# Kernel optimization log

Hardware: AMD Instinct MI355X
Metric: run time of the kernel (lower is better)

## Reference

```python
import jax, jax.numpy as jnp
import numpy as np

N_NODES = 10000
N_EDGES = 200000
STEPS = 2


def setup_inputs() -> dict:
    key = jax.random.key(0)
    ks = jax.random.split(key, 32)

    def w(k, shape):
        return jax.random.normal(k, shape, dtype=jnp.float32) * 0.05

    inp = {
        "x": jax.random.normal(ks[0], (N_NODES, 128), dtype=jnp.float32),
        "edge_attr": jax.random.normal(ks[1], (N_EDGES, 64), dtype=jnp.float32),
        "edge_index": jax.random.randint(ks[2], (2, N_EDGES), 0, N_NODES, dtype=jnp.int32),
        # node embedding MLP: 128 -> 128 -> 128 (ReLU after each, end_with_relu=True)
        "Wne1": w(ks[3], (128, 128)), "bne1": jnp.zeros((128,), jnp.float32),
        "Wne2": w(ks[4], (128, 128)), "bne2": jnp.zeros((128,), jnp.float32),
        # edge embedding MLP: 64 -> 128 -> 128
        "Wee1": w(ks[5], (64, 128)), "bee1": jnp.zeros((128,), jnp.float32),
        "Wee2": w(ks[6], (128, 128)), "bee2": jnp.zeros((128,), jnp.float32),
        # mlp_edge: (2*128*2 + 128*2)=768 -> 512 -> 128, ReLU after each
        "We1": w(ks[7], (768, 512)), "be1": jnp.zeros((512,), jnp.float32),
        "We2": w(ks[8], (512, 128)), "be2": jnp.zeros((128,), jnp.float32),
        # mlp_node: (128*2 + 128)=384 -> 128, ReLU
        "Wn1": w(ks[9], (384, 128)), "bn1": jnp.zeros((128,), jnp.float32),
        # update_mlp: 128 -> 128, ReLU
        "Wu": w(ks[10], (128, 128)), "bu": jnp.zeros((128,), jnp.float32),
        # node classification: 128 -> 128 (ReLU) -> 1
        "Wnc1": w(ks[11], (128, 128)), "bnc1": jnp.zeros((128,), jnp.float32),
        "Wnc2": w(ks[12], (128, 1)), "bnc2": jnp.zeros((1,), jnp.float32),
        # edge classification: 128 -> 128 (ReLU) -> 1
        "Wec1": w(ks[13], (128, 128)), "bec1": jnp.zeros((128,), jnp.float32),
        "Wec2": w(ks[14], (128, 1)), "bec2": jnp.zeros((1,), jnp.float32),
    }
    return inp


def reference(x, edge_attr, edge_index,
              Wne1, bne1, Wne2, bne2,
              Wee1, bee1, Wee2, bee2,
              We1, be1, We2, be2,
              Wn1, bn1, Wu, bu,
              Wnc1, bnc1, Wnc2, bnc2,
              Wec1, bec1, Wec2, bec2):
    relu = jax.nn.relu
    N = x.shape[0]
    j, i = edge_index[0], edge_index[1]  # j = source, i = target

    nf = relu(relu(x @ Wne1 + bne1) @ Wne2 + bne2)            # [N, 128]
    ef = relu(relu(edge_attr @ Wee1 + bee1) @ Wee2 + bee2)    # [E, 128]
    nf0, ef0 = nf, ef

    for _ in range(STEPS):
        # skip connections: concat initial features
        nfc = jnp.concatenate([nf0, nf], axis=1)   # [N, 256]
        efc = jnp.concatenate([ef0, ef], axis=1)   # [E, 256]
        x_i = nfc[i]                               # [E, 256] gather (target)
        x_j = nfc[j]                               # [E, 256] gather (source)
        # mlp_edge on [x_i, x_j, e_ij] -> new edge features [E, 128]
        e = relu(relu(jnp.concatenate([x_i, x_j, efc], axis=1) @ We1 + be1) @ We2 + be2)
        # message: mlp_node on [x_i, edge_attr] -> [E, 128]
        m = relu(jnp.concatenate([x_i, e], axis=1) @ Wn1 + bn1)
        # aggregate (add) messages at target nodes i
        agg = jax.ops.segment_sum(m, i, num_segments=N)       # [N, 128]
        # update MLP
        nf = relu(agg @ Wu + bu)
        ef = e

    preds_node = jnp.squeeze(relu(nf @ Wnc1 + bnc1) @ Wnc2 + bnc2)  # [N]
    preds_edge = jnp.squeeze(relu(ef @ Wec1 + bec1) @ Wec2 + bec2)  # [E]
    return (preds_edge, preds_node)
```

## Files before the change

### kernel.cpp

```cpp
#include <hip/hip_runtime.h>
#include <hip/hip_bf16.h>

#define N_NODES 10000
#define N_EDGES 200000
#define TE 32

typedef __attribute__((ext_vector_type(8))) short short8;
typedef __attribute__((ext_vector_type(4))) float f32x4;

static __device__ __forceinline__ ushort f2bf(float x) {
  union { __hip_bfloat16 h; ushort u; } v;
  v.h = __float2bfloat16(x);
  return v.u;
}
static __device__ __forceinline__ uint pk2bf(float lo, float hi) {
  union { __hip_bfloat162 h; uint u; } v;
  v.h = __float22bfloat162_rn(make_float2(lo, hi));
  return v.u;
}
static __device__ __forceinline__ float bf2f(ushort h) {
  union { uint u; float f; } v; v.u = ((uint)h) << 16;
  return v.f;
}

__device__ __forceinline__ void permute_job(
    const float* W, ushort* Wp, int o, int K, int N, int ld,
    int row0, int n0, int Ntot)
{
  if (o >= K * N) return;
  int k = o & 31;
  int n = (o >> 5) % N;
  int kt = o / (N * 32);
  Wp[(size_t)kt * Ntot * 32 + (size_t)(n0 + n) * 32 + k] =
      f2bf(W[(size_t)(row0 + kt * 32 + k) * ld + n]);
}

__global__ __launch_bounds__(256) void permute_all(
    const float* __restrict__ We1, const float* __restrict__ We2,
    const float* __restrict__ Wn1, const float* __restrict__ Wee1,
    const float* __restrict__ Wee2, const float* __restrict__ Wec1,
    ushort* __restrict__ Wsp, ushort* __restrict__ W1ep,
    ushort* __restrict__ W2p, ushort* __restrict__ W3ep,
    ushort* __restrict__ Wee1p, ushort* __restrict__ Wee2p,
    ushort* __restrict__ Wec1p)
{
  int b = blockIdx.x, t = threadIdx.x;
  if (b < 512)       permute_job(We1, Wsp,  (b       ) * 256 + t, 256, 512, 512,   0,    0, 1152);
  else if (b < 1024) permute_job(We1, Wsp,  (b - 512 ) * 256 + t, 256, 512, 512, 256,  512, 1152);
  else if (b < 1152) permute_job(Wn1, Wsp,  (b - 1024) * 256 + t, 256, 128, 128,   0, 1024, 1152);
  else if (b < 1664) permute_job(We1, W1ep, (b - 1152) * 256 + t, 256, 512, 512, 512,    0,  512);
  else if (b < 1920) permute_job(We2, W2p,  (b - 1664) * 256 + t, 512, 128, 128,   0,    0,  128);
  else if (b < 1984) permute_job(Wn1, W3ep, (b - 1920) * 256 + t, 128, 128, 128, 256,    0,  128);
  else if (b < 2016) permute_job(Wee1, Wee1p,(b - 1984) * 256 + t,  64, 128, 128,   0,    0,  128);
  else if (b < 2080) permute_job(Wee2, Wee2p,(b - 2016) * 256 + t, 128, 128, 128,   0,    0,  128);
  else               permute_job(Wec1, Wec1p,(b - 2080) * 256 + t, 128, 128, 128,   0,    0,  128);
}

__global__ __launch_bounds__(256) void mlp1_kernel(
    const float* __restrict__ in, int n_rows,
    const float* __restrict__ W, const float* __restrict__ b,
    ushort* __restrict__ out)
{
  __shared__ float s_a[8][128];
  const int r0 = blockIdx.x * 8;
  const int t = threadIdx.x;
  for (int idx = t; idx < 8 * 128; idx += 256) {
    int r = idx >> 7, k = idx & 127;
    int row = r0 + r;
    s_a[r][k] = (row < n_rows) ? in[(size_t)row * 128 + k] : 0.f;
  }
  __syncthreads();
  const int c = t & 127;
  const int g = t >> 7;
  float acc[4];
#pragma unroll
  for (int e = 0; e < 4; ++e) acc[e] = b[c];
  for (int k = 0; k < 128; ++k) {
    float w = W[(size_t)k * 128 + c];
#pragma unroll
    for (int e = 0; e < 4; ++e) acc[e] = fmaf(s_a[g * 4 + e][k], w, acc[e]);
  }
#pragma unroll
  for (int e = 0; e < 4; ++e) {
    int row = r0 + g * 4 + e;
    if (row < n_rows) out[(size_t)row * 128 + c] = f2bf(fmaxf(acc[e], 0.f));
  }
}

__global__ __launch_bounds__(256) void embed_all(
    const float* __restrict__ x,
    const float* __restrict__ Wne1, const float* __restrict__ bne1,
    const float* __restrict__ Wne2, const float* __restrict__ bne2,
    const float* __restrict__ edge_attr,
    const ushort* __restrict__ Wee1p, const float* __restrict__ bee1,
    const ushort* __restrict__ Wee2p, const float* __restrict__ bee2,
    ushort* __restrict__ nf0, ushort* __restrict__ nf,
    ushort* __restrict__ ef0)
{
  __shared__ __align__(16) char smem[40960];
  const int t = threadIdx.x;

  if (blockIdx.x < 1250) {
    float* s_a = (float*)smem;
    float* s_h = (float*)(smem + 4096);
    const int r0 = blockIdx.x * 8;
    for (int idx = t; idx < 1024; idx += 256) {
      int r = idx >> 7, k = idx & 127;
      s_a[r * 128 + k] = x[(size_t)(r0 + r) * 128 + k];
    }
    __syncthreads();
    const int c = t & 127, g = t >> 7;
    float acc[4];
#pragma unroll
    for (int e = 0; e < 4; ++e) acc[e] = bne1[c];
    for (int k = 0; k < 128; ++k) {
      float w = Wne1[(size_t)k * 128 + c];
#pragma unroll
      for (int e = 0; e < 4; ++e) acc[e] = fmaf(s_a[(g * 4 + e) * 128 + k], w, acc[e]);
    }
#pragma unroll
    for (int e = 0; e < 4; ++e) s_h[(g * 4 + e) * 128 + c] = fmaxf(acc[e], 0.f);
    __syncthreads();
#pragma unroll
    for (int e = 0; e < 4; ++e) acc[e] = bne2[c];
    for (int k = 0; k < 128; ++k) {
      float w = Wne2[(size_t)k * 128 + c];
#pragma unroll
      for (int e = 0; e < 4; ++e) acc[e] = fmaf(s_h[(g * 4 + e) * 128 + k], w, acc[e]);
    }
#pragma unroll
    for (int e = 0; e < 4; ++e) {
      int row = r0 + g * 4 + e;
      ushort v = f2bf(fmaxf(acc[e], 0.f));
      nf0[(size_t)row * 128 + c] = v;
      nf[(size_t)row * 128 + c] = v;
    }
    return;
  }

  char* s_a = smem;
  char* s_h = smem + 8192;
  ushort* s_o = (ushort*)(smem + 24576);
  const int r0 = (blockIdx.x - 1250) * 64;

  for (int idx = t; idx < 512; idx += 256) {
    int r = idx >> 3, c8 = idx & 7;
    const float* src = edge_attr + (size_t)(r0 + r) * 64 + c8 * 8;
    float4 v0 = *(const float4*)src;
    float4 v1 = *(const float4*)(src + 4);
    uint o4[4] = {pk2bf(v0.x, v0.y), pk2bf(v0.z, v0.w),
                  pk2bf(v1.x, v1.y), pk2bf(v1.z, v1.w)};
    *(uint4*)(s_a + ((r * 128 + c8 * 16) ^ ((r & 7) << 4))) = *(uint4*)o4;
  }
  __syncthreads();

  const int lane = t & 63, wave = t >> 6;
  const int r15 = lane & 15, g = lane >> 4;
  const int swz = (r15 & 7) << 4;
  const int arow = wave * 16 + r15;

  f32x4 h1[8];
#pragma unroll
  for (int j = 0; j < 8; ++j) { float bv = bee1[j * 16 + r15]; h1[j] = (f32x4){bv, bv, bv, bv}; }
#pragma unroll
  for (int kt = 0; kt < 2; ++kt) {
    short8 a = *(const short8*)(s_a + ((arow * 128 + kt * 64 + g * 16) ^ swz));
    const ushort* wk = Wee1p + kt * 4096 + r15 * 32 + g * 8;
#pragma unroll
    for (int j = 0; j < 8; ++j) {
      short8 b = *(const short8*)(wk + j * 512);
      h1[j] = __builtin_amdgcn_mfma_f32_16x16x32_bf16(a, b, h1[j], 0, 0, 0);
    }
  }
#pragma unroll
  for (int j = 0; j < 8; ++j)
#pragma unroll
    for (int r = 0; r < 4; ++r) {
      int row = wave * 16 + g * 4 + r;
      int col = j * 16 + r15;
      *(ushort*)(s_h + ((row * 256 + col * 2) ^ ((row & 7) << 4))) = f2bf(fmaxf(h1[j][r], 0.f));
    }
  __syncthreads();

  f32x4 h2[8];
#pragma unroll
  for (int j = 0; j < 8; ++j) { float bv = bee2[j * 16 + r15]; h2[j] = (f32x4){bv, bv, bv, bv}; }
#pragma unroll
  for (int kt = 0; kt < 4; ++kt) {
    short8 a = *(const short8*)(s_h + ((arow * 256 + kt * 64 + g * 16) ^ swz));
    const ushort* wk = Wee2p + kt * 4096 + r15 * 32 + g * 8;
#pragma unroll
    for (int j = 0; j < 8; ++j) {
      short8 b = *(const short8*)(wk + j * 512);
      h2[j] = __builtin_amdgcn_mfma_f32_16x16x32_bf16(a, b, h2[j], 0, 0, 0);
    }
  }
#pragma unroll
  for (int j = 0; j < 8; ++j)
#pragma unroll
    for (int r = 0; r < 4; ++r) {
      int row = wave * 16 + g * 4 + r;
      s_o[row * 128 + j * 16 + r15] = f2bf(fmaxf(h2[j][r], 0.f));
    }
  __syncthreads();
  for (int idx = t; idx < 1024; idx += 256) {
    int r = idx >> 4, c16 = idx & 15;
    uint4 v = *(uint4*)(&s_o[r * 128 + c16 * 8]);
    *(uint4*)(ef0 + (size_t)(r0 + r) * 128 + c16 * 8) = v;
  }
}

__global__ __launch_bounds__(256) void head_all(
    const ushort* __restrict__ ef,
    const ushort* __restrict__ Wec1p, const float* __restrict__ bec1,
    const float* __restrict__ Wec2, const float* __restrict__ bec2,
    const ushort* __restrict__ nf,
    const float* __restrict__ Wnc1, const float* __restrict__ bnc1,
    const float* __restrict__ Wnc2, const float* __restrict__ bnc2,
    float* __restrict__ preds_edge, float* __restrict__ preds_node)
{
  __shared__ __align__(16) char smem[50176];
  const int t = threadIdx.x;

  if (blockIdx.x < 3125) {
    char* s_a = smem;
    float* s_hf = (float*)(smem + 16384);
    const int r0 = blockIdx.x * 64;
    for (int idx = t; idx < 1024; idx += 256) {
      int r = idx >> 4, c16 = idx & 15;
      uint4 v = *(const uint4*)(ef + (size_t)(r0 + r) * 128 + c16 * 8);
      *(uint4*)(s_a + ((r * 256 + c16 * 16) ^ ((r & 7) << 4))) = v;
    }
    __syncthreads();
    const int lane = t & 63, wave = t >> 6;
    const int r15 = lane & 15, g = lane >> 4;
    const int swz = (r15 & 7) << 4;
    const int arow = wave * 16 + r15;

    f32x4 h1[8];
#pragma unroll
    for (int j = 0; j < 8; ++j) { float bv = bec1[j * 16 + r15]; h1[j] = (f32x4){bv, bv, bv, bv}; }
#pragma unroll
    for (int kt = 0; kt < 4; ++kt) {
      short8 a = *(const short8*)(s_a + ((arow * 256 + kt * 64 + g * 16) ^ swz));
      const ushort* wk = Wec1p + kt * 4096 + r15 * 32 + g * 8;
#pragma unroll
      for (int j = 0; j < 8; ++j) {
        short8 b = *(const short8*)(wk + j * 512);
        h1[j] = __builtin_amdgcn_mfma_f32_16x16x32_bf16(a, b, h1[j], 0, 0, 0);
      }
    }
#pragma unroll
    for (int j = 0; j < 8; ++j)
#pragma unroll
      for (int r = 0; r < 4; ++r) {
        int row = wave * 16 + g * 4 + r;
        s_hf[row * 132 + j * 16 + r15] = fmaxf(h1[j][r], 0.f);
      }
    __syncthreads();
    {
      int row = t >> 2, q = t & 3;
      float p = 0.f;
#pragma unroll
      for (int c = 0; c < 32; ++c) {
        int col = q * 32 + c;
        p = fmaf(s_hf[row * 132 + col], Wec2[col], p);
      }
      p += __shfl_down(p, 1, 64);
      p += __shfl_down(p, 2, 64);
      if (q == 0) preds_edge[r0 + row] = p + bec2[0];
    }
    return;
  }

  float* s_a = (float*)smem;
  float* s_h = (float*)(smem + 4096);
  const int r0 = (blockIdx.x - 3125) * 8;
  for (int idx = t; idx < 1024; idx += 256) {
    int r = idx >> 7, k = idx & 127;
    s_a[r * 128 + k] = bf2f(nf[(size_t)(r0 + r) * 128 + k]);
  }
  __syncthreads();
  const int c = t & 127, g = t >> 7;
  float acc[4];
#pragma unroll
  for (int e = 0; e < 4; ++e) acc[e] = bnc1[c];
  for (int k = 0; k < 128; ++k) {
    float w = Wnc1[(size_t)k * 128 + c];
#pragma unroll
    for (int e = 0; e < 4; ++e) acc[e] = fmaf(s_a[(g * 4 + e) * 128 + k], w, acc[e]);
  }
#pragma unroll
  for (int e = 0; e < 4; ++e) s_h[(g * 4 + e) * 128 + c] = fmaxf(acc[e], 0.f);
  __syncthreads();

  const int wave = t >> 6, lane = t & 63;
#pragma unroll
  for (int e2 = 0; e2 < 2; ++e2) {
    int r = wave * 2 + e2;
    float p = s_h[r * 128 + lane] * Wnc2[lane] + s_h[r * 128 + lane + 64] * Wnc2[lane + 64];
#pragma unroll
    for (int off = 32; off; off >>= 1) p += __shfl_down(p, off, 64);
    if (lane == 0) preds_node[r0 + r] = p + bnc2[0];
  }
}

__global__ __launch_bounds__(256) void prep_all(
    const ushort* __restrict__ nf0, const ushort* __restrict__ nf,
    const ushort* __restrict__ Wsp, ushort* __restrict__ Ppack,
    float* __restrict__ agg)
{
  const int t = threadIdx.x;
  if (blockIdx.x >= 1413) {
    size_t i = (size_t)(blockIdx.x - 1413) * 256 + t;
    ((uint4*)agg)[i] = (uint4){0u, 0u, 0u, 0u};
    return;
  }
  __shared__ char s_a[64 * 512];
  const int bx = blockIdx.x % 157;
  const int r0 = bx * 64;
  const int cc = (blockIdx.x / 157) * 128;

  for (int idx = t; idx < 64 * 32; idx += 256) {
    int r = idx >> 5, c = idx & 31;
    int n = r0 + r; if (n >= N_NODES) n = N_NODES - 1;
    const ushort* base = (c < 16 ? nf0 : nf) + (size_t)n * 128 + (c & 15) * 8;
    *(uint4*)(s_a + ((r * 512 + c * 16) ^ ((r & 7) << 4))) = *(const uint4*)base;
  }
  __syncthreads();

  const int lane = t & 63, wave = t >> 6;
  const int r15 = lane & 15, g = lane >> 4;
  const int swz = (r15 & 7) << 4;

  f32x4 acc[8];
#pragma unroll
  for (int j = 0; j < 8; ++j) acc[j] = (f32x4){0.f, 0.f, 0.f, 0.f};
#pragma unroll
  for (int kt = 0; kt < 8; ++kt) {
    short8 a = *(const short8*)(s_a + (((wave * 16 + r15) * 512 + kt * 64 + g * 16) ^ swz));
    const ushort* wk = Wsp + (size_t)kt * 36864 + (size_t)(cc + r15) * 32 + g * 8;
#pragma unroll
    for (int j = 0; j < 8; ++j) {
      short8 b = *(const short8*)(wk + j * 512);
      acc[j] = __builtin_amdgcn_mfma_f32_16x16x32_bf16(a, b, acc[j], 0, 0, 0);
    }
  }
#pragma unroll
  for (int j = 0; j < 8; ++j)
#pragma unroll
    for (int r = 0; r < 4; ++r) {
      int row = r0 + wave * 16 + g * 4 + r;
      if (row < N_NODES)
        Ppack[(size_t)row * 1152 + cc + j * 16 + r15] = f2bf(acc[j][r]);
    }
}

__global__ __launch_bounds__(512, 4) void fused_edge_mfma(
    const ushort* __restrict__ Ppack,
    const ushort* __restrict__ ef0, const ushort* __restrict__ efA,
    ushort* __restrict__ ef,
    const int* __restrict__ ei,
    const ushort* __restrict__ W1ep, const float* __restrict__ be1,
    const ushort* __restrict__ W2p,  const float* __restrict__ be2,
    const ushort* __restrict__ W3ep, const float* __restrict__ bn1,
    float* __restrict__ agg)
{
  __shared__ __align__(16) char s_a[TE * 512];
  __shared__ __align__(16) char s_h[TE * 1024];
  __shared__ __align__(16) ushort s_q[TE * 136];
  __shared__ int s_i[TE], s_j[TE];

  const int t = threadIdx.x;
  const int NWG = N_EDGES / TE;
  const int q = NWG / 8, rr = NWG % 8;
  int xcd = blockIdx.x & 7, bidx = blockIdx.x >> 3;
  int wgid = (xcd < rr ? xcd * (q + 1) : rr * (q + 1) + (xcd - rr) * q) + bidx;
  const int e0 = wgid * TE;

  if (t < TE) s_j[t] = ei[e0 + t];
  else if (t < 2 * TE) s_i[t - TE] = ei[N_EDGES + e0 + (t - TE)];
  __syncthreads();

  for (int idx = t; idx < TE * 32; idx += 512) {
    int e = idx >> 5, c = idx & 31;
    const ushort* base = (c < 16 ? ef0 : efA) + (size_t)(e0 + e) * 128 + (c & 15) * 8;
    *(uint4*)(s_a + ((e * 512 + c * 16) ^ ((e & 7) << 4))) = *(const uint4*)base;
  }
  for (int idx = t; idx < TE * 64; idx += 512) {
    int e = idx >> 6, c = idx & 63;
    uint4 vi = *(const uint4*)(Ppack + (size_t)s_i[e] * 1152 + c * 8);
    uint4 vj = *(const uint4*)(Ppack + (size_t)s_j[e] * 1152 + 512 + c * 8);
    const ushort* pa = (const ushort*)&vi;
    const ushort* pb = (const ushort*)&vj;
    uint o4[4];
#pragma unroll
    for (int z = 0; z < 4; ++z)
      o4[z] = pk2bf(bf2f(pa[2 * z]) + bf2f(pb[2 * z]),
                    bf2f(pa[2 * z + 1]) + bf2f(pb[2 * z + 1]));
    *(uint4*)(s_h + ((e * 1024 + c * 16) ^ ((e & 7) << 4))) = *(uint4*)o4;
  }
  {
    int e = t >> 4, c = t & 15;
    uint4 v = *(const uint4*)(Ppack + (size_t)s_i[e] * 1152 + 1024 + c * 8);
    *(uint4*)((char*)s_q + e * 272 + c * 16) = v;
  }
  __syncthreads();

  const int lane = t & 63, wave = t >> 6;
  const int r15 = lane & 15, g = lane >> 4;
  const int swz = (r15 & 7) << 4;
  const int wb = wave * 64, wb2 = wave * 16;

  f32x4 acc1[2][4];
#pragma unroll
  for (int j = 0; j < 4; ++j) {
    float bv = be1[wb + j * 16 + r15];
#pragma unroll
    for (int mt = 0; mt < 2; ++mt)
#pragma unroll
      for (int r = 0; r < 4; ++r) {
        int row = mt * 16 + g * 4 + r;
        int col = wb + j * 16 + r15;
        ushort u = *(const ushort*)(s_h + ((row * 1024 + col * 2) ^ ((row & 7) << 4)));
        acc1[mt][j][r] = bv + bf2f(u);
      }
  }
  {
    const ushort* wkb = W1ep + (size_t)(wb + r15) * 32 + g * 8;
    short8 bc[4], bn[4];
#pragma unroll
    for (int j = 0; j < 4; ++j) bc[j] = *(const short8*)(wkb + j * 512);
    for (int kt = 0; kt < 8; ++kt) {
      short8 a0 = *(const short8*)(s_a + ((r15 * 512 + kt * 64 + g * 16) ^ swz));
      short8 a1 = *(const short8*)(s_a + (((r15 + 16) * 512 + kt * 64 + g * 16) ^ swz));
      const ushort* wnx = wkb + (size_t)(kt + 1) * 16384;
#pragma unroll
      for (int j = 0; j < 4; ++j) bn[j] = *(const short8*)(wnx + j * 512);
#pragma unroll
      for (int j = 0; j < 4; ++j) {
        acc1[0][j] = __builtin_amdgcn_mfma_f32_16x16x32_bf16(a0, bc[j], acc1[0][j], 0, 0, 0);
        acc1[1][j] = __builtin_amdgcn_mfma_f32_16x16x32_bf16(a1, bc[j], acc1[1][j], 0, 0, 0);
      }
#pragma unroll
      for (int j = 0; j < 4; ++j) bc[j] = bn[j];
    }
  }
#pragma unroll
  for (int mt = 0; mt < 2; ++mt)
#pragma unroll
    for (int j = 0; j < 4; ++j)
#pragma unroll
      for (int r = 0; r < 4; ++r) {
        int row = mt * 16 + g * 4 + r;
        int col = wb + j * 16 + r15;
        *(ushort*)(s_h + ((row * 1024 + col * 2) ^ ((row & 7) << 4))) =
            f2bf(fmaxf(acc1[mt][j][r], 0.f));
      }
  __syncthreads();

  f32x4 acc2[2], acc2b[2];
  {
    float bv = be2[wb2 + r15];
    acc2[0] = (f32x4){bv, bv, bv, bv};
    acc2[1] = (f32x4){bv, bv, bv, bv};
    acc2b[0] = (f32x4){0.f, 0.f, 0.f, 0.f};
    acc2b[1] = (f32x4){0.f, 0.f, 0.f, 0.f};
  }
  {
    const ushort* wkb = W2p + (size_t)(wb2 + r15) * 32 + g * 8;
    short8 bA = *(const short8*)(wkb);
    short8 bB = *(const short8*)(wkb + 4096);
    for (int kt2 = 0; kt2 < 8; ++kt2) {
      int ab0 = (2 * kt2) * 64 + g * 16;
      int ab1 = ab0 + 64;
      short8 a0e = *(const short8*)(s_h + ((r15 * 1024 + ab0) ^ swz));
      short8 a1e = *(const short8*)(s_h + (((r15 + 16) * 1024 + ab0) ^ swz));
      short8 a0o = *(const short8*)(s_h + ((r15 * 1024 + ab1) ^ swz));
      short8 a1o = *(const short8*)(s_h + (((r15 + 16) * 1024 + ab1) ^ swz));
      short8 bAn = *(const short8*)(wkb + (size_t)(2 * kt2 + 2) * 4096);
      short8 bBn = *(const short8*)(wkb + (size_t)(2 * kt2 + 3) * 4096);
      acc2[0]  = __builtin_amdgcn_mfma_f32_16x16x32_bf16(a0e, bA, acc2[0], 0, 0, 0);
      acc2b[0] = __builtin_amdgcn_mfma_f32_16x16x32_bf16(a0o, bB, acc2b[0], 0, 0, 0);
      acc2[1]  = __builtin_amdgcn_mfma_f32_16x16x32_bf16(a1e, bA, acc2[1], 0, 0, 0);
      acc2b[1] = __builtin_amdgcn_mfma_f32_16x16x32_bf16(a1o, bB, acc2b[1], 0, 0, 0);
      bA = bAn; bB = bBn;
    }
    acc2[0] = acc2[0] + acc2b[0];
    acc2[1] = acc2[1] + acc2b[1];
  }
#pragma unroll
  for (int mt = 0; mt < 2; ++mt)
#pragma unroll
    for (int r = 0; r < 4; ++r) {
      int row = mt * 16 + g * 4 + r;
      int col = wb2 + r15;
      *(ushort*)(s_a + ((row * 512 + col * 2) ^ ((row & 7) << 4))) =
          f2bf(fmaxf(acc2[mt][r], 0.f));
    }
  __syncthreads();

  {
    int e = t >> 4, c = t & 15;
    uint4 v = *(const uint4*)(s_a + ((e * 512 + c * 16) ^ ((e & 7) << 4)));
    *(uint4*)(ef + (size_t)(e0 + e) * 128 + c * 8) = v;
  }

  f32x4 acc3[2];
  {
    float bv = bn1[wb2 + r15];
#pragma unroll
    for (int mt = 0; mt < 2; ++mt)
#pragma unroll
      for (int r = 0; r < 4; ++r) {
        int row = mt * 16 + g * 4 + r;
        acc3[mt][r] = bv + bf2f(s_q[row * 136 + wb2 + r15]);
      }
  }
  {
    const ushort* w3b = W3ep + (size_t)(wb2 + r15) * 32 + g * 8;
    short8 bq[4];
#pragma unroll
    for (int kk = 0; kk < 4; ++kk) bq[kk] = *(const short8*)(w3b + (size_t)kk * 4096);
#pragma unroll
    for (int kk = 0; kk < 4; ++kk) {
      short8 a0 = *(const short8*)(s_a + ((r15 * 512 + kk * 64 + g * 16) ^ swz));
      short8 a1 = *(const short8*)(s_a + (((r15 + 16) * 512 + kk * 64 + g * 16) ^ swz));
      acc3[0] = __builtin_amdgcn_mfma_f32_16x16x32_bf16(a0, bq[kk], acc3[0], 0, 0, 0);
      acc3[1] = __builtin_amdgcn_mfma_f32_16x16x32_bf16(a1, bq[kk], acc3[1], 0, 0, 0);
    }
  }
#pragma unroll
  for (int mt = 0; mt < 2; ++mt)
#pragma unroll
    for (int r = 0; r < 4; ++r) {
      int row = mt * 16 + g * 4 + r;
      int node = s_i[row];
      atomicAdd(&agg[(size_t)node * 128 + wb2 + r15], fmaxf(acc3[mt][r], 0.f));
    }
}

extern "C" void kernel_launch(void* const* d_in, const int* in_sizes, int n_in,
                              void* d_out, int out_size, void* d_ws, size_t ws_size,
                              hipStream_t stream) {
  const float* x         = (const float*)d_in[0];
  const float* edge_attr = (const float*)d_in[1];
  const int*   ei        = (const int*)d_in[2];
  const float* Wne1 = (const float*)d_in[3];  const float* bne1 = (const float*)d_in[4];
  const float* Wne2 = (const float*)d_in[5];  const float* bne2 = (const float*)d_in[6];
  const float* Wee1 = (const float*)d_in[7];  const float* bee1 = (const float*)d_in[8];
  const float* Wee2 = (const float*)d_in[9];  const float* bee2 = (const float*)d_in[10];
  const float* We1  = (const float*)d_in[11]; const float* be1  = (const float*)d_in[12];
  const float* We2  = (const float*)d_in[13]; const float* be2  = (const float*)d_in[14];
  const float* Wn1  = (const float*)d_in[15]; const float* bn1  = (const float*)d_in[16];
  const float* Wu   = (const float*)d_in[17]; const float* bu   = (const float*)d_in[18];
  const float* Wnc1 = (const float*)d_in[19]; const float* bnc1 = (const float*)d_in[20];
  const float* Wnc2 = (const float*)d_in[21]; const float* bnc2 = (const float*)d_in[22];
  const float* Wec1 = (const float*)d_in[23]; const float* bec1 = (const float*)d_in[24];
  const float* Wec2 = (const float*)d_in[25]; const float* bec2 = (const float*)d_in[26];

  float* preds_edge = (float*)d_out;
  float* preds_node = preds_edge + N_EDGES;

  char* w = (char*)d_ws;
  ushort* nf0  = (ushort*)w; w += (size_t)N_NODES * 128 * 2;
  ushort* nf   = (ushort*)w; w += (size_t)N_NODES * 128 * 2;
  ushort* ef0  = (ushort*)w; w += (size_t)N_EDGES * 128 * 2;
  ushort* ef   = (ushort*)w; w += (size_t)N_EDGES * 128 * 2;
  float*  agg  = (float*)w;  w += (size_t)N_NODES * 128 * 4;
  ushort* Ppack = (ushort*)w; w += (size_t)N_NODES * 1152 * 2;
  ushort* Wsp  = (ushort*)w; w += (size_t)8 * 1152 * 32 * 2;
  ushort* W1ep = (ushort*)w; w += (size_t)9 * 512 * 32 * 2;
  ushort* W2p  = (ushort*)w; w += (size_t)18 * 128 * 32 * 2;
  ushort* W3ep = (ushort*)w; w += (size_t)4 * 128 * 32 * 2;
  ushort* Wee1p = (ushort*)w; w += (size_t)64 * 128 * 2;
  ushort* Wee2p = (ushort*)w; w += (size_t)128 * 128 * 2;
  ushort* Wec1p = (ushort*)w; w += (size_t)128 * 128 * 2;

  permute_all<<<2144, 256, 0, stream>>>(
      We1, We2, Wn1, Wee1, Wee2, Wec1,
      Wsp, W1ep, W2p, W3ep, Wee1p, Wee2p, Wec1p);

  embed_all<<<1250 + 3125, 256, 0, stream>>>(
      x, Wne1, bne1, Wne2, bne2,
      edge_attr, Wee1p, bee1, Wee2p, bee2, nf0, nf, ef0);

  for (int s = 0; s < 2; ++s) {
    prep_all<<<1413 + 1250, 256, 0, stream>>>(nf0, nf, Wsp, Ppack, agg);
    fused_edge_mfma<<<N_EDGES / TE, 512, 0, stream>>>(
        Ppack, ef0, (s == 0 ? ef0 : ef), ef, ei,
        W1ep, be1, W2p, be2, W3ep, bn1, agg);
    mlp1_kernel<<<(N_NODES + 7) / 8, 256, 0, stream>>>(agg, N_NODES, Wu, bu, nf);
  }

  head_all<<<3125 + 1250, 256, 0, stream>>>(
      ef, Wec1p, bec1, Wec2, bec2,
      nf, Wnc1, bnc1, Wnc2, bnc2, preds_edge, preds_node);
}
```

Measured before the change: 654.3 us.

## Privatize scatter-add buffers per XCD and fuse final node update into edge head

The edge kernel now scatters messages into one of eight private aggregation buffers, chosen by the block's XCD index, instead of a single shared buffer. The goal is to cut cross-die atomic contention and coherence traffic on the segment-sum. Consumers sum the eight partial buffers when they read them. The second step's node update MLP is moved into the edge-head kernel so it runs alongside the edge classifier, and a separate node-classification kernel follows. In exchange, the zeroing work grows eightfold (more zeroing blocks, four stores per thread) and the consumers must read eight copies.

```diff
diff --git a/kernel.cpp b/kernel.cpp
--- a/kernel.cpp
+++ b/kernel.cpp
@@ -4,6 +4,7 @@
 #define N_NODES 10000
 #define N_EDGES 200000
 #define TE 32
+#define NN128 ((size_t)N_NODES * 128)
 
 typedef __attribute__((ext_vector_type(8))) short short8;
 typedef __attribute__((ext_vector_type(4))) float f32x4;
@@ -57,7 +58,7 @@
 }
 
 __global__ __launch_bounds__(256) void mlp1_kernel(
-    const float* __restrict__ in, int n_rows,
+    const float* __restrict__ agg8, int n_rows,
     const float* __restrict__ W, const float* __restrict__ b,
     ushort* __restrict__ out)
 {
@@ -67,7 +68,13 @@
   for (int idx = t; idx < 8 * 128; idx += 256) {
     int r = idx >> 7, k = idx & 127;
     int row = r0 + r;
-    s_a[r][k] = (row < n_rows) ? in[(size_t)row * 128 + k] : 0.f;
+    float s = 0.f;
+    if (row < n_rows) {
+#pragma unroll
+      for (int c = 0; c < 8; ++c)
+        s += agg8[(size_t)c * NN128 + (size_t)row * 128 + k];
+    }
+    s_a[r][k] = s;
   }
   __syncthreads();
   const int c = t & 127;
@@ -210,14 +217,14 @@
   }
 }
 
-__global__ __launch_bounds__(256) void head_all(
+__global__ __launch_bounds__(256) void tail_all(
     const ushort* __restrict__ ef,
     const ushort* __restrict__ Wec1p, const float* __restrict__ bec1,
     const float* __restrict__ Wec2, const float* __restrict__ bec2,
-    const ushort* __restrict__ nf,
-    const float* __restrict__ Wnc1, const float* __restrict__ bnc1,
-    const float* __restrict__ Wnc2, const float* __restrict__ bnc2,
-    float* __restrict__ preds_edge, float* __restrict__ preds_node)
+    const float* __restrict__ agg8,
+    const float* __restrict__ Wu, const float* __restrict__ bu,
+    ushort* __restrict__ nf,
+    float* __restrict__ preds_edge)
 {
   __shared__ __align__(16) char smem[50176];
   const int t = threadIdx.x;
@@ -274,46 +281,87 @@
   }
 
   float* s_a = (float*)smem;
-  float* s_h = (float*)(smem + 4096);
   const int r0 = (blockIdx.x - 3125) * 8;
   for (int idx = t; idx < 1024; idx += 256) {
     int r = idx >> 7, k = idx & 127;
-    s_a[r * 128 + k] = bf2f(nf[(size_t)(r0 + r) * 128 + k]);
+    int row = r0 + r;
+    float s = 0.f;
+    if (row < N_NODES) {
+#pragma unroll
+      for (int c = 0; c < 8; ++c)
+        s += agg8[(size_t)c * NN128 + (size_t)row * 128 + k];
+    }
+    s_a[r * 128 + k] = s;
   }
   __syncthreads();
   const int c = t & 127, g = t >> 7;
   float acc[4];
 #pragma unroll
-  for (int e = 0; e < 4; ++e) acc[e] = bnc1[c];
+  for (int e = 0; e < 4; ++e) acc[e] = bu[c];
   for (int k = 0; k < 128; ++k) {
-    float w = Wnc1[(size_t)k * 128 + c];
+    float w = Wu[(size_t)k * 128 + c];
 #pragma unroll
     for (int e = 0; e < 4; ++e) acc[e] = fmaf(s_a[(g * 4 + e) * 128 + k], w, acc[e]);
   }
 #pragma unroll
-  for (int e = 0; e < 4; ++e) s_h[(g * 4 + e) * 128 + c] = fmaxf(acc[e], 0.f);
+  for (int e = 0; e < 4; ++e) {
+    int row = r0 + g * 4 + e;
+    if (row < N_NODES) nf[(size_t)row * 128 + c] = f2bf(fmaxf(acc[e], 0.f));
+  }
+}
+
+__global__ __launch_bounds__(256) void node_cls(
+    const ushort* __restrict__ feat,
+    const float* __restrict__ W1, const float* __restrict__ b1,
+    const float* __restrict__ W2, const float* __restrict__ b2,
+    float* __restrict__ out)
+{
+  __shared__ float s_a[8][128];
+  __shared__ float s_h[8][128];
+  const int r0 = blockIdx.x * 8;
+  const int t = threadIdx.x;
+  for (int idx = t; idx < 8 * 128; idx += 256) {
+    int r = idx >> 7, k = idx & 127;
+    s_a[r][k] = bf2f(feat[(size_t)(r0 + r) * 128 + k]);
+  }
+  __syncthreads();
+  const int c = t & 127;
+  const int g = t >> 7;
+  float acc[4];
+#pragma unroll
+  for (int e = 0; e < 4; ++e) acc[e] = b1[c];
+  for (int k = 0; k < 128; ++k) {
+    float w = W1[(size_t)k * 128 + c];
+#pragma unroll
+    for (int e = 0; e < 4; ++e) acc[e] = fmaf(s_a[g * 4 + e][k], w, acc[e]);
+  }
+#pragma unroll
+  for (int e = 0; e < 4; ++e) s_h[g * 4 + e][c] = fmaxf(acc[e], 0.f);
   __syncthreads();
 
   const int wave = t >> 6, lane = t & 63;
 #pragma unroll
   for (int e2 = 0; e2 < 2; ++e2) {
     int r = wave * 2 + e2;
-    float p = s_h[r * 128 + lane] * Wnc2[lane] + s_h[r * 128 + lane + 64] * Wnc2[lane + 64];
+    float p = s_h[r][lane] * W2[lane] + s_h[r][lane + 64] * W2[lane + 64];
 #pragma unroll
     for (int off = 32; off; off >>= 1) p += __shfl_down(p, off, 64);
-    if (lane == 0) preds_node[r0 + r] = p + bnc2[0];
+    if (lane == 0) out[r0 + r] = p + b2[0];
   }
 }
 
 __global__ __launch_bounds__(256) void prep_all(
     const ushort* __restrict__ nf0, const ushort* __restrict__ nf,
     const ushort* __restrict__ Wsp, ushort* __restrict__ Ppack,
-    float* __restrict__ agg)
+    float* __restrict__ agg8)
 {
   const int t = threadIdx.x;
   if (blockIdx.x >= 1413) {
-    size_t i = (size_t)(blockIdx.x - 1413) * 256 + t;
-    ((uint4*)agg)[i] = (uint4){0u, 0u, 0u, 0u};
+    uint4* a4 = (uint4*)agg8;
+    size_t base = (size_t)(blockIdx.x - 1413) * 1024;
+#pragma unroll
+    for (int it = 0; it < 4; ++it)
+      a4[base + it * 256 + t] = (uint4){0u, 0u, 0u, 0u};
     return;
   }
   __shared__ char s_a[64 * 512];
@@ -364,7 +412,7 @@
     const ushort* __restrict__ W1ep, const float* __restrict__ be1,
     const ushort* __restrict__ W2p,  const float* __restrict__ be2,
     const ushort* __restrict__ W3ep, const float* __restrict__ bn1,
-    float* __restrict__ agg)
+    float* __restrict__ agg8)
 {
   __shared__ __align__(16) char s_a[TE * 512];
   __shared__ __align__(16) char s_h[TE * 1024];
@@ -372,6 +420,7 @@
   __shared__ int s_i[TE], s_j[TE];
 
   const int t = threadIdx.x;
+  float* agg = agg8 + (size_t)(blockIdx.x & 7) * NN128;
   const int NWG = N_EDGES / TE;
   const int q = NWG / 8, rr = NWG % 8;
   int xcd = blockIdx.x & 7, bidx = blockIdx.x >> 3;
@@ -567,7 +616,7 @@
   ushort* nf   = (ushort*)w; w += (size_t)N_NODES * 128 * 2;
   ushort* ef0  = (ushort*)w; w += (size_t)N_EDGES * 128 * 2;
   ushort* ef   = (ushort*)w; w += (size_t)N_EDGES * 128 * 2;
-  float*  agg  = (float*)w;  w += (size_t)N_NODES * 128 * 4;
+  float*  agg8 = (float*)w;  w += (size_t)8 * NN128 * 4;
   ushort* Ppack = (ushort*)w; w += (size_t)N_NODES * 1152 * 2;
   ushort* Wsp  = (ushort*)w; w += (size_t)8 * 1152 * 32 * 2;
   ushort* W1ep = (ushort*)w; w += (size_t)9 * 512 * 32 * 2;
@@ -585,15 +634,17 @@
       x, Wne1, bne1, Wne2, bne2,
       edge_attr, Wee1p, bee1, Wee2p, bee2, nf0, nf, ef0);
 
-  for (int s = 0; s < 2; ++s) {
-    prep_all<<<1413 + 1250, 256, 0, stream>>>(nf0, nf, Wsp, Ppack, agg);
-    fused_edge_mfma<<<N_EDGES / TE, 512, 0, stream>>>(
-        Ppack, ef0, (s == 0 ? ef0 : ef), ef, ei,
-        W1ep, be1, W2p, be2, W3ep, bn1, agg);
-    mlp1_kernel<<<(N_NODES + 7) / 8, 256, 0, stream>>>(agg, N_NODES, Wu, bu, nf);
-  }
-
-  head_all<<<3125 + 1250, 256, 0, stream>>>(
-      ef, Wec1p, bec1, Wec2, bec2,
-      nf, Wnc1, bnc1, Wnc2, bnc2, preds_edge, preds_node);
-}
+  prep_all<<<1413 + 2500, 256, 0, stream>>>(nf0, nf, Wsp, Ppack, agg8);
+  fused_edge_mfma<<<N_EDGES / TE, 512, 0, stream>>>(
+      Ppack, ef0, ef0, ef, ei, W1ep, be1, W2p, be2, W3ep, bn1, agg8);
+  mlp1_kernel<<<(N_NODES + 7) / 8, 256, 0, stream>>>(agg8, N_NODES, Wu, bu, nf);
+
+  prep_all<<<1413 + 2500, 256, 0, stream>>>(nf0, nf, Wsp, Ppack, agg8);
+  fused_edge_mfma<<<N_EDGES / TE, 512, 0, stream>>>(
+      Ppack, ef0, ef, ef, ei, W1ep, be1, W2p, be2, W3ep, bn1, agg8);
+  tail_all<<<3125 + 1250, 256, 0, stream>>>(
+      ef, Wec1p, bec1, Wec2, bec2, agg8, Wu, bu, nf, preds_edge);
+
+  node_cls<<<(N_NODES + 7) / 8, 256, 0, stream>>>(
+      nf, Wnc1, bnc1, Wnc2, bnc2, preds_node);
+}
```

Measured after the change: 663.9 us. No clear change (+1.5%).
